# Optimization experiments

Hardware: AMD Instinct MI355X
Metric: run time of the kernel (lower is better)

The kernel has to match this reference:

```python
import jax, jax.numpy as jnp
import numpy as np

DIM = 1024
HEADS = 16
HEAD_DIM = DIM // HEADS
SCALE = DIM ** (-0.5)  # NOTE: module scales by full dim, not head dim


def setup_inputs() -> dict:
    key = jax.random.key(0)
    k1, k2, k3, k4 = jax.random.split(key, 4)
    x = jax.random.normal(k1, (4, 2048, DIM), dtype=jnp.float32)
    w_qkv = jax.random.normal(k2, (DIM, 3 * DIM), dtype=jnp.float32) * (DIM ** -0.5)
    w_out = jax.random.normal(k3, (DIM, DIM), dtype=jnp.float32) * (DIM ** -0.5)
    b_out = jax.random.normal(k4, (DIM,), dtype=jnp.float32) * 0.01
    return {"x": x, "w_qkv": w_qkv, "w_out": w_out, "b_out": b_out}


def reference(x, w_qkv, w_out, b_out):
    b, n, _ = x.shape
    qkv = x @ w_qkv  # [b, n, 3*dim]
    # 'b n (qkv h d) -> qkv b h n d'
    qkv = qkv.reshape(b, n, 3, HEADS, HEAD_DIM).transpose(2, 0, 3, 1, 4)
    q, k, v = qkv[0], qkv[1], qkv[2]  # each [b, h, n, d]
    dots = jnp.einsum('bhid,bhjd->bhij', q, k) * SCALE
    attn = jax.nn.softmax(dots, axis=-1)
    out = jnp.einsum('bhij,bhjd->bhid', attn, v)
    out = out.transpose(0, 2, 1, 3).reshape(b, n, DIM)  # 'b h n d -> b n (h d)'
    return out @ w_out + b_out
```

## Files before the change

### kernel.cpp

```cpp
#include <hip/hip_runtime.h>
#include <math.h>

#define BATCH 4
#define SEQ   2048
#define DMODEL 1024
#define HEADS 16
#define DHEAD 64
#define SCALE 0.03125f
#define KEXP  0.045084220027780106f
#define QKV_ELEMS (BATCH * HEADS * SEQ * DHEAD)

typedef __attribute__((ext_vector_type(8))) short short8;
typedef __attribute__((ext_vector_type(4))) float floatx4;
typedef unsigned int u32;

__device__ __forceinline__ unsigned short f2bf(float f) {
  union { float f; unsigned u; } v;
  v.f = f;
  return (unsigned short)((v.u + 0x7FFFu + ((v.u >> 16) & 1u)) >> 16);
}

__device__ __forceinline__ float fast_exp2(float x) {
#if __has_builtin(__builtin_amdgcn_exp2f)
  return __builtin_amdgcn_exp2f(x);
#else
  return __expf(x * 0.6931471805599453f);
#endif
}

__device__ __forceinline__ u32 pack_bf16(float p0, float p1) {
#if __has_builtin(__builtin_amdgcn_cvt_pk_bf16_f32)
  typedef __bf16 bf16x2 __attribute__((ext_vector_type(2)));
  bf16x2 t = __builtin_amdgcn_cvt_pk_bf16_f32(p0, p1);
  u32 r;
  __builtin_memcpy(&r, &t, 4);
  return r;
#else
  u32 a0 = __float_as_uint(p0) + 0x8000u;
  u32 a1 = __float_as_uint(p1) + 0x8000u;
  return __builtin_amdgcn_perm(a1, a0, 0x07060302);
#endif
}

__device__ __forceinline__ void async_ld16(const void* g, void* l) {
  __builtin_amdgcn_global_load_lds(
      (const __attribute__((address_space(1))) u32*)g,
      (__attribute__((address_space(3))) u32*)l, 16, 0, 0);
}

__device__ __forceinline__ void trans_tile(const float* __restrict__ W,
                                           unsigned short* __restrict__ WT,
                                           int K, int N, int n0, int k0,
                                           float (*tile)[33]) {
  const int tx = threadIdx.x & 31, ty = threadIdx.x >> 5;
#pragma unroll
  for (int i = 0; i < 4; ++i)
    tile[ty + i * 8][tx] = W[(size_t)(k0 + ty + i * 8) * N + n0 + tx];
  __syncthreads();
#pragma unroll
  for (int i = 0; i < 4; ++i)
    WT[(size_t)(n0 + ty + i * 8) * K + k0 + tx] = f2bf(tile[tx][ty + i * 8]);
}

__global__ __launch_bounds__(256) void prep_kernel(
    const float* __restrict__ x, const float* __restrict__ wqkv,
    const float* __restrict__ wout, unsigned short* __restrict__ xb,
    unsigned short* __restrict__ wqkvT, unsigned short* __restrict__ woutT) {
  __shared__ float tile[32][33];
  const int bx = blockIdx.x;
  if (bx < 8192) {
    size_t i = ((size_t)bx * 256 + threadIdx.x) * 4;
    float4 v = *(const float4*)(x + i);
    ushort4 o;
    o.x = f2bf(v.x); o.y = f2bf(v.y); o.z = f2bf(v.z); o.w = f2bf(v.w);
    *(ushort4*)(xb + i) = o;
  } else if (bx < 11264) {
    int t = bx - 8192;
    trans_tile(wqkv, wqkvT, 1024, 3072, (t % 96) * 32, (t / 96) * 32, tile);
  } else {
    int t = bx - 11264;
    trans_tile(wout, woutT, 1024, 1024, (t % 32) * 32, (t / 32) * 32, tile);
  }
}

#define G_BAR() __builtin_amdgcn_s_barrier()
#define G_LGKM0() asm volatile("s_waitcnt lgkmcnt(0)" ::: "memory")

#define STAGE_TILE(t)                                                          \
  do {                                                                         \
    const unsigned short* Ab =                                                 \
        A + (size_t)(m0 + srow) * 1024 + (t) * 64 + schunk * 8;                \
    const unsigned short* Bb =                                                 \
        BT + (size_t)(n0 + srow) * 1024 + (t) * 64 + schunk * 8;               \
    unsigned short* sa = smemS + ((t) % 3) * 24576;                            \
    unsigned short* sb = sa + 16384;                                           \
    async_ld16(Ab, sa + tid * 8);                                              \
    async_ld16(Ab + 64 * 1024, sa + 4096 + tid * 8);                           \
    async_ld16(Ab + 128 * 1024, sa + 8192 + tid * 8);                          \
    async_ld16(Ab + 192 * 1024, sa + 12288 + tid * 8);                         \
    async_ld16(Bb, sb + tid * 8);                                              \
    async_ld16(Bb + 64 * 1024, sb + 4096 + tid * 8);                           \
  } while (0)

#define RD_A(SAp, mh)                                                          \
  do {                                                                         \
    _Pragma("unroll") for (int mi = 0; mi < 4; ++mi) {                         \
      a[mi][0] = *(const short8*)((SAp) + rowA + (mh)*4096 + mi * 1024 + cof0);\
      a[mi][1] = *(const short8*)((SAp) + rowA + (mh)*4096 + mi * 1024 + cof1);\
    }                                                                          \
  } while (0)

#define RD_B(SBp)                                                              \
  do {                                                                         \
    _Pragma("unroll") for (int ni = 0; ni < 2; ++ni) {                         \
      b[ni][0] = *(const short8*)((SBp) + rowB + ni * 1024 + cof0);            \
      b[ni][1] = *(const short8*)((SBp) + rowB + ni * 1024 + cof1);            \
    }                                                                          \
  } while (0)

#define CLUSTER(mh)                                                            \
  do {                                                                         \
    __builtin_amdgcn_s_setprio(1);                                             \
    _Pragma("unroll") for (int mi = 0; mi < 4; ++mi) {                         \
      _Pragma("unroll") for (int ni = 0; ni < 2; ++ni) {                       \
        acc[(mh)*4 + mi][ni] = __builtin_amdgcn_mfma_f32_16x16x32_bf16(        \
            a[mi][0], b[ni][0], acc[(mh)*4 + mi][ni], 0, 0, 0);                \
        acc[(mh)*4 + mi][ni] = __builtin_amdgcn_mfma_f32_16x16x32_bf16(        \
            a[mi][1], b[ni][1], acc[(mh)*4 + mi][ni], 0, 0, 0);                \
      }                                                                        \
    }                                                                          \
    __builtin_amdgcn_s_setprio(0);                                             \
  } while (0)

__device__ __forceinline__ void core256x128(
    const unsigned short* __restrict__ A, const unsigned short* __restrict__ BT,
    unsigned short* smemS, int m0, int n0, floatx4 (&acc)[8][2]) {
  const int tid = threadIdx.x;
  const int wave = tid >> 6, lane = tid & 63;
  const int Q4 = lane >> 4, L = lane & 15;
  const int wr = wave >> 2, wc = wave & 3;
  const int srow = tid >> 3;
  const int schunk = (tid & 7) ^ (srow & 7);
  const int xorL = L & 7;
  const int cof0 = (Q4 ^ xorL) * 8;
  const int cof1 = ((4 + Q4) ^ xorL) * 8;
  const int rowA = wr * 8192 + L * 64;
  const int rowB = wc * 2048 + L * 64;

  short8 a[4][2], b[2][2];
#pragma unroll
  for (int mt = 0; mt < 8; ++mt)
#pragma unroll
    for (int nt = 0; nt < 2; ++nt) acc[mt][nt] = (floatx4){0.f, 0.f, 0.f, 0.f};

  STAGE_TILE(0);
  STAGE_TILE(1);
  asm volatile("s_waitcnt vmcnt(6)" ::: "memory");
  G_BAR();

#pragma unroll
  for (int u = 0; u < 16; ++u) {
    unsigned short* SA = smemS + (u % 3) * 24576;
    unsigned short* SB = SA + 16384;
    RD_A(SA, 0);
    RD_B(SB);
    if (u + 2 < 16) STAGE_TILE(u + 2);
    G_BAR(); G_LGKM0();
    CLUSTER(0);
    G_BAR();
    RD_A(SA, 1);
    G_BAR(); G_LGKM0();
    CLUSTER(1);
    if (u + 2 < 16) asm volatile("s_waitcnt vmcnt(6)" ::: "memory");
    else            asm volatile("s_waitcnt vmcnt(0)" ::: "memory");
    G_BAR();
  }
}

__global__ __launch_bounds__(512, 2) void gemm_qkv_kernel(
    const unsigned short* __restrict__ A, const unsigned short* __restrict__ BT,
    unsigned short* __restrict__ qk, unsigned short* __restrict__ vtg) {
  __shared__ __align__(16) unsigned char smem[147456];
  unsigned short* smemS = (unsigned short*)smem;

  const int tid = threadIdx.x;
  const int wave = tid >> 6, lane = tid & 63;
  const int Q4 = lane >> 4, L = lane & 15;
  const int wr = wave >> 2, wc = wave & 3;

  const int flat = blockIdx.y * 24 + blockIdx.x;
  const int swz = (flat & 7) * 96 + (flat >> 3);
  const int mblk = swz / 24, nblk = swz % 24;
  const int m0 = mblk * 256, n0 = nblk * 128;

  floatx4 acc[8][2];
  core256x128(A, BT, smemS, m0, n0, acc);

  const int bb = m0 >> 11;
  const int ntok0 = m0 & 2047;
  unsigned short* T = smemS;

  if (nblk < 16) {
    const float qsc = (nblk < 8) ? KEXP : 1.0f;
    unsigned short* dst = qk + (size_t)(nblk >> 3) * QKV_ELEMS;
    const int h0 = (nblk & 7) * 2;
#pragma unroll
    for (int mt = 0; mt < 8; ++mt)
#pragma unroll
      for (int nt = 0; nt < 2; ++nt) {
        const int col = wc * 32 + nt * 16 + L;
        const int tokl = wr * 128 + mt * 16 + Q4 * 4;
#pragma unroll
        for (int r = 0; r < 4; ++r)
          T[(tokl + r) * 136 + col] = f2bf(acc[mt][nt][r] * qsc);
      }
    __syncthreads();
#pragma unroll
    for (int it2 = 0; it2 < 8; ++it2) {
      int slot = it2 * 512 + tid;
      int tok = slot >> 4, ch = slot & 15;
      int hh = ch >> 3, inner = ch & 7;
      *(short8*)(dst +
                 (((size_t)((bb * 16 + h0 + hh) * 2048 + ntok0 + tok)) << 6) +
                 inner * 8) = *(const short8*)&T[tok * 136 + hh * 64 + inner * 8];
    }
  } else {
    const int nv0 = (nblk - 16) * 128;
#pragma unroll
    for (int mt = 0; mt < 8; ++mt)
#pragma unroll
      for (int nt = 0; nt < 2; ++nt) {
        const int col = wc * 32 + nt * 16 + L;
#pragma unroll
        for (int r = 0; r < 4; ++r) {
          int tok = wr * 128 + mt * 16 + Q4 * 4 + r;
          int pcm = (tok & ~31) | ((tok & 15) << 1) | ((tok >> 4) & 1);
          T[col * 264 + pcm] = f2bf(acc[mt][nt][r]);
        }
      }
    __syncthreads();
#pragma unroll
    for (int it2 = 0; it2 < 8; ++it2) {
      int slot = it2 * 512 + tid;
      int col = slot >> 5, ch = slot & 31;
      int nc = nv0 + col;
      *(short8*)(vtg +
                 (((size_t)((bb * 16 + (nc >> 6)) * 64 + (nc & 63))) << 11) +
                 ntok0 + ch * 8) = *(const short8*)&T[col * 264 + ch * 8];
    }
  }
}

__global__ __launch_bounds__(512, 2) void gemm_out_kernel(
    const unsigned short* __restrict__ A, const unsigned short* __restrict__ BT,
    const float* __restrict__ bias, float* __restrict__ C) {
  __shared__ __align__(16) unsigned char smem[147456];
  unsigned short* smemS = (unsigned short*)smem;

  const int tid = threadIdx.x;
  const int wave = tid >> 6, lane = tid & 63;
  const int Q4 = lane >> 4, L = lane & 15;
  const int wr = wave >> 2, wc = wave & 3;

  const int flat = blockIdx.y * 8 + blockIdx.x;
  const int swz = (flat & 7) * 32 + (flat >> 3);
  const int m0 = (swz >> 3) * 256, n0 = (swz & 7) * 128;

  floatx4 acc[8][2];
  core256x128(A, BT, smemS, m0, n0, acc);

#pragma unroll
  for (int mt = 0; mt < 8; ++mt) {
#pragma unroll
    for (int nt = 0; nt < 2; ++nt) {
      int nc = n0 + wc * 32 + nt * 16 + L;
      float bv = bias[nc];
#pragma unroll
      for (int r = 0; r < 4; ++r) {
        int m = m0 + wr * 128 + mt * 16 + Q4 * 4 + r;
        C[(size_t)m * DMODEL + nc] = acc[mt][nt][r] + bv;
      }
    }
  }
}

#undef STAGE_TILE
#undef RD_A
#undef RD_B
#undef CLUSTER
#undef G_BAR
#undef G_LGKM0

__global__ __launch_bounds__(512, 4) void attn_kernel(
    const unsigned short* __restrict__ Qb, const unsigned short* __restrict__ Kb,
    const unsigned short* __restrict__ Vtg, unsigned short* __restrict__ Op) {
  __shared__ __align__(16) unsigned short Ks[2][64 * 64];
  __shared__ __align__(16) unsigned short Vs[2][64 * 64];
  const int tid = threadIdx.x;
  const int wave = tid >> 6, lane = tid & 63;
  const int quad = lane >> 4, l16 = lane & 15;
  const int bh = blockIdx.x & 63, qt = blockIdx.x >> 6;
  const size_t base = (size_t)bh * SEQ * DHEAD;
  const int lrow = lane >> 3, ls = lane & 7;
  const int dblk = ls ^ (lrow & 7);
  const int sw = l16 & 7;

  const unsigned short* kbase = Kb + base;
  const unsigned short* vbase = Vtg + base;
  const int rowS = wave * 8 + lrow;

  short8 onesf;
#pragma unroll
  for (int i = 0; i < 8; ++i) onesf[i] = (short)0x3F80;

  short8 qf[2][2];
#pragma unroll
  for (int qs = 0; qs < 2; ++qs) {
    int qrow = qt * 256 + wave * 32 + qs * 16 + l16;
    qf[qs][0] = *(const short8*)(Qb + base + (size_t)qrow * DHEAD + quad * 8);
    qf[qs][1] =
        *(const short8*)(Qb + base + (size_t)qrow * DHEAD + 32 + quad * 8);
  }

  floatx4 o[2][4], lacc[2];
#pragma unroll
  for (int qs = 0; qs < 2; ++qs) {
    lacc[qs] = (floatx4){0.f, 0.f, 0.f, 0.f};
#pragma unroll
    for (int dt = 0; dt < 4; ++dt) o[qs][dt] = (floatx4){0.f, 0.f, 0.f, 0.f};
  }

#define STAGE(buf, kc)                                                         \
  do {                                                                         \
    async_ld16(kbase + (size_t)((kc)*64 + rowS) * DHEAD + dblk * 8,            \
               &Ks[buf][wave * 512]);                                          \
    async_ld16(vbase + (size_t)rowS * SEQ + (kc)*64 + dblk * 8,                \
               &Vs[buf][wave * 512]);                                          \
  } while (0)

#define COMPUTE(buf)                                                           \
  do {                                                                         \
    _Pragma("unroll") for (int kc2 = 0; kc2 < 2; ++kc2) {                      \
      const int krow = kc2 * 32;                                               \
      short8 kf00 =                                                            \
          *(short8*)(&Ks[buf][0] + (krow + l16) * 64 + ((quad ^ sw) * 8));     \
      short8 kf01 = *(short8*)(&Ks[buf][0] + (krow + l16) * 64 +               \
                               (((4 + quad) ^ sw) * 8));                       \
      short8 kf10 = *(short8*)(&Ks[buf][0] + (krow + 16 + l16) * 64 +          \
                               ((quad ^ sw) * 8));                             \
      short8 kf11 = *(short8*)(&Ks[buf][0] + (krow + 16 + l16) * 64 +          \
                               (((4 + quad) ^ sw) * 8));                       \
      short8 vf[4];                                                            \
      _Pragma("unroll") for (int dt = 0; dt < 4; ++dt) vf[dt] =                \
          *(short8*)(&Vs[buf][0] + (dt * 16 + l16) * 64 +                      \
                     (((kc2 * 4 + quad) ^ sw) * 8));                           \
      floatx4 s0[2], s1[2];                                                    \
      _Pragma("unroll") for (int qs = 0; qs < 2; ++qs) {                       \
        s0[qs] = (floatx4){0.f, 0.f, 0.f, 0.f};                                \
        s1[qs] = (floatx4){0.f, 0.f, 0.f, 0.f};                                \
        s0[qs] = __builtin_amdgcn_mfma_f32_16x16x32_bf16(kf00, qf[qs][0],      \
                                                         s0[qs], 0, 0, 0);     \
        s0[qs] = __builtin_amdgcn_mfma_f32_16x16x32_bf16(kf01, qf[qs][1],      \
                                                         s0[qs], 0, 0, 0);     \
        s1[qs] = __builtin_amdgcn_mfma_f32_16x16x32_bf16(kf10, qf[qs][0],      \
                                                         s1[qs], 0, 0, 0);     \
        s1[qs] = __builtin_amdgcn_mfma_f32_16x16x32_bf16(kf11, qf[qs][1],      \
                                                         s1[qs], 0, 0, 0);     \
      }                                                                        \
      short8 pf[2];                                                            \
      _Pragma("unroll") for (int qs = 0; qs < 2; ++qs) {                       \
        union { short8 s8; u32 u[4]; } pu;                                     \
        _Pragma("unroll") for (int r = 0; r < 4; ++r) {                        \
          pu.u[r] = pack_bf16(fast_exp2(s0[qs][r]), fast_exp2(s1[qs][r]));     \
        }                                                                      \
        pf[qs] = pu.s8;                                                        \
      }                                                                        \
      _Pragma("unroll") for (int qs = 0; qs < 2; ++qs) {                       \
        lacc[qs] = __builtin_amdgcn_mfma_f32_16x16x32_bf16(pf[qs], onesf,      \
                                                           lacc[qs], 0, 0, 0); \
        _Pragma("unroll") for (int dt = 0; dt < 4; ++dt) o[qs][dt] =           \
            __builtin_amdgcn_mfma_f32_16x16x32_bf16(pf[qs], vf[dt],            \
                                                    o[qs][dt], 0, 0, 0);       \
      }                                                                        \
    }                                                                          \
  } while (0)

  STAGE(0, 0);
  for (int kc = 0; kc < SEQ / 64; kc += 2) {
    __syncthreads();
    if (kc + 1 < SEQ / 64) STAGE(1, kc + 1);
    COMPUTE(0);
    __syncthreads();
    if (kc + 2 < SEQ / 64) STAGE(0, kc + 2);
    COMPUTE(1);
  }
#undef STAGE
#undef COMPUTE

  const int b = bh >> 4, h = bh & 15;
#pragma unroll
  for (int qs = 0; qs < 2; ++qs) {
#pragma unroll
    for (int r = 0; r < 4; ++r) {
      float inv = 1.f / lacc[qs][r];
      int n = qt * 256 + wave * 32 + qs * 16 + quad * 4 + r;
      size_t rowbase = ((size_t)(b * SEQ + n)) * DMODEL + h * DHEAD;
#pragma unroll
      for (int dt = 0; dt < 4; ++dt)
        Op[rowbase + dt * 16 + l16] = f2bf(o[qs][dt][r] * inv);
    }
  }
}

extern "C" void kernel_launch(void* const* d_in, const int* in_sizes, int n_in,
                              void* d_out, int out_size, void* d_ws,
                              size_t ws_size, hipStream_t stream) {
  const float* x = (const float*)d_in[0];
  const float* w_qkv = (const float*)d_in[1];
  const float* w_out = (const float*)d_in[2];
  const float* b_out = (const float*)d_in[3];
  float* out = (float*)d_out;

  unsigned short* ws = (unsigned short*)d_ws;
  unsigned short* xb = ws;
  unsigned short* wqkvT = xb + 8388608;
  unsigned short* woutT = wqkvT + 3145728;
  unsigned short* qb = woutT + 1048576;
  unsigned short* kb = qb + QKV_ELEMS;
  unsigned short* vtg = kb + QKV_ELEMS;
  unsigned short* op = vtg + QKV_ELEMS;

  prep_kernel<<<dim3(12288), dim3(256), 0, stream>>>(x, w_qkv, w_out, xb,
                                                     wqkvT, woutT);
  gemm_qkv_kernel<<<dim3(24, 32), dim3(512), 0, stream>>>(xb, wqkvT, qb, vtg);
  attn_kernel<<<dim3(512), dim3(512), 0, stream>>>(qb, kb, vtg, op);
  gemm_out_kernel<<<dim3(8, 32), dim3(512), 0, stream>>>(op, woutT, b_out, out);
}
```

Before: 248.4 us.

## Use K=32 pipelined core in QKV GEMM to halve LDS and raise occupancy

Replaces the QKV GEMM main loop with a new core that stages 32-wide K tiles in a triple-buffered LDS ring. This cuts shared memory per block from 144KB to 72KB, and launch bounds rise from 2 to 4 blocks per CU. The new loop loads all A/B fragments, then issues MFMAs at raised wave priority, with one barrier pair per K step. It trades more loop iterations and barriers for higher occupancy and better latency hiding; the epilogue still reuses smem, and register pressure at 4 blocks per CU may cause spills.

```diff
diff --git a/kernel.cpp b/kernel.cpp
--- a/kernel.cpp
+++ b/kernel.cpp
@@ -177,16 +177,79 @@
   }
 }
 
-__global__ __launch_bounds__(512, 2) void gemm_qkv_kernel(
+#define K32_STAGE(t)                                                           \
+  do {                                                                         \
+    const unsigned short* Ab =                                                 \
+        A + (size_t)(m0 + rA) * 1024 + (t) * 32 + cS;                          \
+    const unsigned short* Bb =                                                 \
+        BT + (size_t)(n0 + rA) * 1024 + (t) * 32 + cS;                         \
+    unsigned short* sa = smemS + ((t) % 3) * 12288;                            \
+    unsigned short* sb = sa + 8192;                                            \
+    async_ld16(Ab, sa + tid * 8);                                              \
+    async_ld16(Ab + 128 * 1024, sa + 4096 + tid * 8);                          \
+    async_ld16(Bb, sb + tid * 8);                                              \
+  } while (0)
+
+__device__ __forceinline__ void core256x128_k32(
     const unsigned short* __restrict__ A, const unsigned short* __restrict__ BT,
-    unsigned short* __restrict__ qk, unsigned short* __restrict__ vtg) {
-  __shared__ __align__(16) unsigned char smem[147456];
-  unsigned short* smemS = (unsigned short*)smem;
-
+    unsigned short* smemS, int m0, int n0, floatx4 (&acc)[8][2]) {
   const int tid = threadIdx.x;
   const int wave = tid >> 6, lane = tid & 63;
   const int Q4 = lane >> 4, L = lane & 15;
   const int wr = wave >> 2, wc = wave & 3;
+  const int rA = tid >> 2;
+  const int cS = ((tid & 3) ^ (rA & 3)) * 8;
+  const int xq = (Q4 ^ (L & 3)) * 8;
+  const int rowA = wr * 4096 + L * 32;
+  const int rowB = wc * 1024 + L * 32;
+
+  short8 a[8], b[2];
+#pragma unroll
+  for (int mt = 0; mt < 8; ++mt)
+#pragma unroll
+    for (int nt = 0; nt < 2; ++nt) acc[mt][nt] = (floatx4){0.f, 0.f, 0.f, 0.f};
+
+  K32_STAGE(0);
+  K32_STAGE(1);
+  asm volatile("s_waitcnt vmcnt(3)" ::: "memory");
+  G_BAR();
+
+#pragma unroll
+  for (int u = 0; u < 32; ++u) {
+    unsigned short* SA = smemS + (u % 3) * 12288;
+    unsigned short* SB = SA + 8192;
+#pragma unroll
+    for (int mt = 0; mt < 8; ++mt)
+      a[mt] = *(const short8*)(SA + rowA + mt * 512 + xq);
+#pragma unroll
+    for (int nt = 0; nt < 2; ++nt)
+      b[nt] = *(const short8*)(SB + rowB + nt * 512 + xq);
+    if (u + 2 < 32) K32_STAGE(u + 2);
+    G_BAR(); G_LGKM0();
+    __builtin_amdgcn_s_setprio(1);
+#pragma unroll
+    for (int mt = 0; mt < 8; ++mt)
+#pragma unroll
+      for (int nt = 0; nt < 2; ++nt)
+        acc[mt][nt] = __builtin_amdgcn_mfma_f32_16x16x32_bf16(
+            a[mt], b[nt], acc[mt][nt], 0, 0, 0);
+    __builtin_amdgcn_s_setprio(0);
+    if (u + 2 < 32) asm volatile("s_waitcnt vmcnt(3)" ::: "memory");
+    else            asm volatile("s_waitcnt vmcnt(0)" ::: "memory");
+    G_BAR();
+  }
+}
+
+__global__ __launch_bounds__(512, 4) void gemm_qkv_kernel(
+    const unsigned short* __restrict__ A, const unsigned short* __restrict__ BT,
+    unsigned short* __restrict__ qk, unsigned short* __restrict__ vtg) {
+  __shared__ __align__(16) unsigned char smem[73728];
+  unsigned short* smemS = (unsigned short*)smem;
+
+  const int tid = threadIdx.x;
+  const int wave = tid >> 6, lane = tid & 63;
+  const int Q4 = lane >> 4, L = lane & 15;
+  const int wr = wave >> 2, wc = wave & 3;
 
   const int flat = blockIdx.y * 24 + blockIdx.x;
   const int swz = (flat & 7) * 96 + (flat >> 3);
@@ -194,7 +257,7 @@
   const int m0 = mblk * 256, n0 = nblk * 128;
 
   floatx4 acc[8][2];
-  core256x128(A, BT, smemS, m0, n0, acc);
+  core256x128_k32(A, BT, smemS, m0, n0, acc);
 
   const int bb = m0 >> 11;
   const int ntok0 = m0 & 2047;
@@ -288,6 +351,7 @@
 #undef RD_A
 #undef RD_B
 #undef CLUSTER
+#undef K32_STAGE
 #undef G_BAR
 #undef G_LGKM0
 
```

Result: faster. 241.7 us (-2.7%).
